# Optimization experiments

Measured on AMD Instinct MI355X. Metric: run time of the kernel, lower is better.

## Reference

```python
import jax, jax.numpy as jnp
import numpy as np

N_NODES = 100000
N_EDGES = 640000
D_IN = 128
HIDDEN = 256
OUT = 256
NUM_GRAPHS = 256


def setup_inputs() -> dict:
    key = jax.random.key(0)
    ks = jax.random.split(key, 8)
    x = jax.random.normal(ks[0], (N_NODES, D_IN), dtype=jnp.float32)
    edge_index = jax.random.randint(ks[1], (2, N_EDGES), 0, N_NODES, dtype=jnp.int64)
    batch = jnp.sort(jax.random.randint(ks[2], (N_NODES,), 0, NUM_GRAPHS, dtype=jnp.int64))
    s1 = 1.0 / np.sqrt(D_IN)
    s2 = 1.0 / np.sqrt(HIDDEN)
    W1_l = jax.random.normal(ks[3], (D_IN, HIDDEN), dtype=jnp.float32) * s1
    W1_r = jax.random.normal(ks[4], (D_IN, HIDDEN), dtype=jnp.float32) * s1
    b1 = jnp.zeros((HIDDEN,), dtype=jnp.float32)
    W2_l = jax.random.normal(ks[5], (HIDDEN, OUT), dtype=jnp.float32) * s2
    W2_r = jax.random.normal(ks[6], (HIDDEN, OUT), dtype=jnp.float32) * s2
    b2 = jnp.zeros((OUT,), dtype=jnp.float32)
    return {"x": x, "edge_index": edge_index, "batch": batch,
            "W1_l": W1_l, "b1": b1, "W1_r": W1_r,
            "W2_l": W2_l, "b2": b2, "W2_r": W2_r}


def _sage_conv(x, src, dst, W_l, b_l, W_r):
    # PyG SAGEConv, aggr='mean': lin_l(mean_{j in N(i)} x_j) + lin_r(x_i)
    n = x.shape[0]
    msgs = x[src]                                              # [E, d] gather
    agg = jax.ops.segment_sum(msgs, dst, num_segments=n)       # [N, d] scatter-add
    cnt = jax.ops.segment_sum(jnp.ones((src.shape[0],), x.dtype), dst, num_segments=n)
    mean = agg / jnp.maximum(cnt, 1.0)[:, None]
    return mean @ W_l + b_l + x @ W_r


def reference(x, edge_index, batch, W1_l, b1, W1_r, W2_l, b2, W2_r):
    src, dst = edge_index[0], edge_index[1]
    h = jax.nn.relu(_sage_conv(x, src, dst, W1_l, b1, W1_r))
    h = _sage_conv(h, src, dst, W2_l, b2, W2_r)
    # global_add_pool: segment sum over per-node graph ids
    return jax.ops.segment_sum(h, batch, num_segments=NUM_GRAPHS)  # [G, OUT]
```

## Files before the change

kernel.cpp:

```cpp
#include <hip/hip_runtime.h>

#define NN 100000
#define NE 640000
#define DIN 128
#define DH 256
#define DOUT 256
#define NG 256
#define NB1 ((NN + 255) / 256)

#define PECH 157
#define CPE (4 * PECH)
#define PEB ((NE + CPE - 1) / CPE)
#define GSP 8

#define PNB 1024
#define CHN2 ((NN + PNB - 1) / PNB)

#define BCH 4096
#define BNB ((NE + BCH - 1) / BCH)

typedef __bf16 bf16_t;
typedef __bf16 bf16x8 __attribute__((ext_vector_type(8)));
typedef __bf16 bf16x2 __attribute__((ext_vector_type(2)));
typedef float f32x4 __attribute__((ext_vector_type(4)));
typedef float f32v2 __attribute__((ext_vector_type(2)));

#if __has_builtin(__builtin_amdgcn_cvt_pk_fp8_f32) && __has_builtin(__builtin_amdgcn_cvt_pk_f32_fp8)
#define USE_HW_FP8 1
#else
#define USE_HW_FP8 0
#endif

#if !USE_HW_FP8
__device__ __forceinline__ unsigned f32_to_fp8_1(float f) {
  unsigned sg = (__float_as_uint(f) >> 31) << 7;
  float af = fabsf(f);
  unsigned body;
  if (af < 0.015625f) {
    body = (unsigned)(int)rintf(af * 512.0f);
  } else {
    unsigned bits = __float_as_uint(af);
    unsigned rb = bits + 0x7FFFFu + ((bits >> 20) & 1u);
    unsigned e = rb >> 23;
    body = ((e - 120u) << 3) | ((rb >> 20) & 7u);
  }
  return (sg | body) & 0xffu;
}
__device__ __forceinline__ float fp8_to_f32_1(unsigned b) {
  unsigned s = b >> 7, e = (b >> 3) & 15u, m = b & 7u;
  float v = (e == 0) ? (float)m * 0.001953125f
                     : __uint_as_float(((e + 120u) << 23) | (m << 20));
  return s ? -v : v;
}
#endif

__device__ __forceinline__ unsigned pack4_fp8(float v0, float v1, float v2, float v3) {
#if USE_HW_FP8
  int u = __builtin_amdgcn_cvt_pk_fp8_f32(v0, v1, 0, false);
  u = __builtin_amdgcn_cvt_pk_fp8_f32(v2, v3, u, true);
  return (unsigned)u;
#else
  return f32_to_fp8_1(v0) | (f32_to_fp8_1(v1) << 8) |
         (f32_to_fp8_1(v2) << 16) | (f32_to_fp8_1(v3) << 24);
#endif
}

__device__ __forceinline__ void unpack4_fp8(unsigned v, float* o) {
#if USE_HW_FP8
  f32v2 a = __builtin_amdgcn_cvt_pk_f32_fp8((int)v, false);
  f32v2 b = __builtin_amdgcn_cvt_pk_f32_fp8((int)v, true);
  o[0] = a[0]; o[1] = a[1]; o[2] = b[0]; o[3] = b[1];
#else
  o[0] = fp8_to_f32_1(v & 0xffu);         o[1] = fp8_to_f32_1((v >> 8) & 0xffu);
  o[2] = fp8_to_f32_1((v >> 16) & 0xffu); o[3] = fp8_to_f32_1(v >> 24);
#endif
}

__device__ __forceinline__ void unpack2_fp8(unsigned v, float* o) {
#if USE_HW_FP8
  f32v2 a = __builtin_amdgcn_cvt_pk_f32_fp8((int)v, false);
  o[0] = a[0]; o[1] = a[1];
#else
  o[0] = fp8_to_f32_1(v & 0xffu); o[1] = fp8_to_f32_1((v >> 8) & 0xffu);
#endif
}

__global__ void k_xcast(const float* __restrict__ x, bf16_t* __restrict__ xb,
                        unsigned char* __restrict__ xf8) {
  size_t i = ((size_t)blockIdx.x * 256 + threadIdx.x) * 8;
  if (i >= (size_t)NN * DIN) return;
  float4 a = *(const float4*)(x + i), b = *(const float4*)(x + i + 4);
  bf16x8 o;
  o[0] = (bf16_t)a.x; o[1] = (bf16_t)a.y; o[2] = (bf16_t)a.z; o[3] = (bf16_t)a.w;
  o[4] = (bf16_t)b.x; o[5] = (bf16_t)b.y; o[6] = (bf16_t)b.z; o[7] = (bf16_t)b.w;
  *(bf16x8*)(xb + i) = o;
  uint2 p;
  p.x = pack4_fp8(a.x, a.y, a.z, a.w);
  p.y = pack4_fp8(b.x, b.y, b.z, b.w);
  *(uint2*)(xf8 + i) = p;
}

__global__ void k_count(const int* __restrict__ dst, int* __restrict__ cnt) {
  int e = blockIdx.x * 256 + threadIdx.x;
  if (e < NE) atomicAdd(&cnt[dst[e]], 1);
}

__global__ void k_scan1(const int* __restrict__ cnt, int* __restrict__ rowptr,
                        int* __restrict__ part) {
  __shared__ int s[256];
  int t = threadIdx.x, i = blockIdx.x * 256 + t;
  int v = (i < NN) ? cnt[i] : 0;
  s[t] = v; __syncthreads();
#pragma unroll
  for (int off = 1; off < 256; off <<= 1) {
    int u = (t >= off) ? s[t - off] : 0;
    __syncthreads();
    s[t] += u;
    __syncthreads();
  }
  if (i < NN) rowptr[i] = s[t] - v;
  if (t == 255) part[blockIdx.x] = s[255];
}

__global__ void k_scan2(int* __restrict__ part) {
  __shared__ int s[512];
  int t = threadIdx.x;
  int v = (t < NB1) ? part[t] : 0;
  s[t] = v; __syncthreads();
#pragma unroll
  for (int off = 1; off < 512; off <<= 1) {
    int u = (t >= off) ? s[t - off] : 0;
    __syncthreads();
    s[t] += u;
    __syncthreads();
  }
  if (t < NB1) part[t] = s[t] - v;
}

__global__ void k_scan3(int* __restrict__ rowptr, const int* __restrict__ part) {
  int i = blockIdx.x * 256 + threadIdx.x;
  if (i < NN) rowptr[i] += part[i >> 8];
  if (i == 0) rowptr[NN] = NE;
}

__global__ void k_gstart2(const int* __restrict__ batch, const int* __restrict__ rowptr,
                          int* __restrict__ gstart, unsigned* __restrict__ wg) {
  int n = blockIdx.x * 256 + threadIdx.x;
  if (n >= NN) return;
  int b = batch[n];
  int prev = (n == 0) ? -1 : batch[n - 1];
  for (int g = prev + 1; g <= b; ++g) gstart[g] = n;
  if (n == NN - 1) {
    for (int g = b + 1; g <= NG; ++g) gstart[g] = NN;
  }
  int e0 = rowptr[n], e1 = rowptr[n + 1];
  unsigned val = ((unsigned)b << 16) | (unsigned)(e1 - e0);
  for (int e = e0; e < e1; ++e) wg[e] = val;
}

__global__ void k_bucket(const int* __restrict__ src, const int* __restrict__ dst,
                         const int* __restrict__ rowptr, int* __restrict__ fill,
                         int* __restrict__ col) {
  int cls = blockIdx.x & 7;
  int cb = blockIdx.x >> 3;
  int e0 = cb * BCH;
  int e1 = (e0 + BCH < NE) ? e0 + BCH : NE;
  for (int e = e0 + threadIdx.x; e < e1; e += 256) {
    int d = dst[e];
    if (((d >> 4) & 7) == cls) {
      int p = rowptr[d] + atomicAdd(&fill[d], 1);
      col[p] = src[e];
    }
  }
}

__global__ void k_agg1(const int* __restrict__ rowptr, const int* __restrict__ col,
                       const unsigned char* __restrict__ xf8, bf16_t* __restrict__ ag1) {
  int w = (blockIdx.x * 256 + threadIdx.x) >> 6;
  int lane = threadIdx.x & 63;
  if (w >= NN) return;
  w = __builtin_amdgcn_readfirstlane(w);
  int e0 = rowptr[w], e1 = rowptr[w + 1];
  float a0 = 0.f, a1 = 0.f;
  int e = e0;
  for (; e + 4 <= e1; e += 4) {
    int s0 = col[e], s1 = col[e + 1], s2 = col[e + 2], s3 = col[e + 3];
    unsigned v0 = *(const unsigned short*)(xf8 + (size_t)s0 * DIN + lane * 2);
    unsigned v1 = *(const unsigned short*)(xf8 + (size_t)s1 * DIN + lane * 2);
    unsigned v2 = *(const unsigned short*)(xf8 + (size_t)s2 * DIN + lane * 2);
    unsigned v3 = *(const unsigned short*)(xf8 + (size_t)s3 * DIN + lane * 2);
    float o[2];
    unpack2_fp8(v0, o); a0 += o[0]; a1 += o[1];
    unpack2_fp8(v1, o); a0 += o[0]; a1 += o[1];
    unpack2_fp8(v2, o); a0 += o[0]; a1 += o[1];
    unpack2_fp8(v3, o); a0 += o[0]; a1 += o[1];
  }
  for (; e < e1; ++e) {
    int s0 = col[e];
    unsigned v0 = *(const unsigned short*)(xf8 + (size_t)s0 * DIN + lane * 2);
    float o[2];
    unpack2_fp8(v0, o); a0 += o[0]; a1 += o[1];
  }
  float r = (e1 > e0) ? __builtin_amdgcn_rcpf((float)(e1 - e0)) : 0.f;
  bf16x2 ov;
  ov[0] = (bf16_t)(a0 * r); ov[1] = (bf16_t)(a1 * r);
  ((bf16x2*)ag1)[(size_t)w * 64 + lane] = ov;
}

__global__ void k_pack1(const float* __restrict__ Wl, const float* __restrict__ Wr,
                        bf16_t* __restrict__ Bp) {
  int t = blockIdx.x * 256 + threadIdx.x;
  if (t >= 8192) return;
  int lane = t & 63, nt = (t >> 6) & 15, kc = t >> 10;
  int n = nt * 16 + (lane & 15);
  int k0 = kc * 32 + (lane >> 4) * 8;
  bf16_t* o = Bp + ((size_t)(kc * 16 + nt) * 64 + lane) * 8;
  for (int j = 0; j < 8; ++j) {
    int k = k0 + j;
    float v = (k < 128) ? Wl[k * 256 + n] : Wr[(k - 128) * 256 + n];
    o[j] = (bf16_t)v;
  }
}

__launch_bounds__(256, 4)
__global__ void k_gemm1(const bf16_t* __restrict__ xb, const bf16_t* __restrict__ ag1,
                        const float* __restrict__ b1,
                        const bf16_t* __restrict__ Bp, unsigned char* __restrict__ hf8) {
  __shared__ unsigned char smem[64 * 512];
  int n0 = blockIdx.x * 64;
  int tid = threadIdx.x;
  {
    int row = tid >> 2, part = tid & 3;
    int node = n0 + row;
    unsigned sw = (row & 7) << 4;
    const uint4* ap = (const uint4*)(ag1 + (size_t)node * DIN);
    const uint4* xp = (const uint4*)(xb + (size_t)node * DIN);
#pragma unroll
    for (int i = 0; i < 4; ++i) {
      int mi = i * 4 + part;
      uint4 va = {0u, 0u, 0u, 0u}, vx = {0u, 0u, 0u, 0u};
      if (node < NN) { va = ap[mi]; vx = xp[mi]; }
      *(uint4*)(smem + row * 512 + (((unsigned)(mi * 16)) ^ sw)) = va;
      *(uint4*)(smem + row * 512 + ((unsigned)(256 + mi * 16) ^ sw)) = vx;
    }
  }
  __syncthreads();
  int wave = tid >> 6, lane = tid & 63, lhi = lane >> 4, llo = lane & 15;
  f32x4 acc[4][4] = {};
  const bf16x8* bptr = (const bf16x8*)Bp;
#pragma unroll
  for (int kc = 0; kc < 8; ++kc) {
    bf16x8 a[4], b[4];
#pragma unroll
    for (int mi = 0; mi < 4; ++mi) {
      int row = mi * 16 + llo;
      unsigned cb = ((unsigned)((kc * 32 + lhi * 8) * 2)) ^ ((row & 7) << 4);
      a[mi] = *(const bf16x8*)(smem + row * 512 + cb);
    }
#pragma unroll
    for (int ni = 0; ni < 4; ++ni)
      b[ni] = bptr[(kc * 16 + wave * 4 + ni) * 64 + lane];
#pragma unroll
    for (int mi = 0; mi < 4; ++mi)
#pragma unroll
      for (int ni = 0; ni < 4; ++ni)
        acc[mi][ni] = __builtin_amdgcn_mfma_f32_16x16x32_bf16(a[mi], b[ni], acc[mi][ni], 0, 0, 0);
  }
  float bias[4];
#pragma unroll
  for (int ni = 0; ni < 4; ++ni) bias[ni] = b1[wave * 64 + ni * 16 + llo];
#pragma unroll
  for (int mi = 0; mi < 4; ++mi)
#pragma unroll
    for (int j = 0; j < 4; ++j) {
      int node = n0 + mi * 16 + lhi * 4 + j;
      if (node < NN) {
        float v0 = fmaxf(acc[mi][0][j] + bias[0], 0.f);
        float v1 = fmaxf(acc[mi][1][j] + bias[1], 0.f);
        float v2 = fmaxf(acc[mi][2][j] + bias[2], 0.f);
        float v3 = fmaxf(acc[mi][3][j] + bias[3], 0.f);
        unsigned u = pack4_fp8(v0, v1, v2, v3);
        *(unsigned*)(hf8 + (size_t)node * 256 + wave * 64 + llo * 4) = u;
      }
    }
}

__global__ void k_poolE2(const int* __restrict__ col, const unsigned* __restrict__ wg,
                         const unsigned char* __restrict__ hf8, float* __restrict__ Y1) {
  __shared__ float gbuf[GSP][256];
  int tid = threadIdx.x;
  int c0 = blockIdx.x * CPE;
  int c1 = (c0 + CPE < NE) ? c0 + CPE : NE;
  if (c0 >= c1) return;
  int gmin = (int)(wg[c0] >> 16), gmax = (int)(wg[c1 - 1] >> 16);
  bool ldsok = (gmax - gmin) < GSP;
  for (int i = tid; i < GSP * 256; i += 256) (&gbuf[0][0])[i] = 0.f;
  __syncthreads();
  int wv = tid >> 6, lane = tid & 63;
  int e0 = __builtin_amdgcn_readfirstlane(c0 + wv * PECH);
  int e1 = e0 + PECH; if (e1 > c1) e1 = c1;
  int dmb = ((lane >> 4) << 6) | (lane & 15);
  float acc[4] = {0.f, 0.f, 0.f, 0.f};
  int curg = -1;
#define EFLUSH() do { if (curg >= 0) {                                        \
    if (ldsok) { float* gp = gbuf[curg - gmin];                               \
      atomicAdd(gp + (dmb | 0),  acc[0]); atomicAdd(gp + (dmb | 16), acc[1]); \
      atomicAdd(gp + (dmb | 32), acc[2]); atomicAdd(gp + (dmb | 48), acc[3]); \
    } else { float* yp = Y1 + (size_t)curg * 256;                             \
      unsafeAtomicAdd(yp + (dmb | 0),  acc[0]);                               \
      unsafeAtomicAdd(yp + (dmb | 16), acc[1]);                               \
      unsafeAtomicAdd(yp + (dmb | 32), acc[2]);                               \
      unsafeAtomicAdd(yp + (dmb | 48), acc[3]); }                             \
    acc[0] = acc[1] = acc[2] = acc[3] = 0.f; } } while (0)
  if (e0 < e1) {
    int e = e0;
    for (; e + 8 <= e1; e += 8) {
      int cv[8]; unsigned wvv[8]; unsigned hv[8];
#pragma unroll
      for (int i = 0; i < 8; ++i) { cv[i] = col[e + i]; wvv[i] = wg[e + i]; }
#pragma unroll
      for (int i = 0; i < 8; ++i)
        hv[i] = *(const unsigned*)(hf8 + (size_t)cv[i] * 256 + lane * 4);
#pragma unroll
      for (int i = 0; i < 8; ++i) {
        int g = (int)(wvv[i] >> 16);
        if (g != curg) { EFLUSH(); curg = g; }
        float w = __builtin_amdgcn_rcpf((float)(wvv[i] & 0xffffu));
        float o[4]; unpack4_fp8(hv[i], o);
        acc[0] += w * o[0]; acc[1] += w * o[1];
        acc[2] += w * o[2]; acc[3] += w * o[3];
      }
    }
    for (; e < e1; ++e) {
      int c = col[e]; unsigned wv2 = wg[e];
      unsigned hvv = *(const unsigned*)(hf8 + (size_t)c * 256 + lane * 4);
      int g = (int)(wv2 >> 16);
      if (g != curg) { EFLUSH(); curg = g; }
      float w = __builtin_amdgcn_rcpf((float)(wv2 & 0xffffu));
      float o[4]; unpack4_fp8(hvv, o);
      acc[0] += w * o[0]; acc[1] += w * o[1];
      acc[2] += w * o[2]; acc[3] += w * o[3];
    }
    EFLUSH();
  }
#undef EFLUSH
  __syncthreads();
  if (ldsok) {
    int ng = gmax - gmin + 1;
    for (int gi = 0; gi < ng; ++gi)
      unsafeAtomicAdd(&Y1[(size_t)(gmin + gi) * 256 + tid], gbuf[gi][tid]);
  }
}

__global__ void k_poolN(const int* __restrict__ batch, const unsigned char* __restrict__ hf8,
                        float* __restrict__ Y2) {
  __shared__ float gbuf[GSP][256];
  int tid = threadIdx.x;
  int n0 = blockIdx.x * CHN2;
  int n1 = (n0 + CHN2 < NN) ? n0 + CHN2 : NN;
  if (n0 >= n1) return;
  int gmin = batch[n0], gmax = batch[n1 - 1];
  bool ldsok = (gmax - gmin) < GSP;
  for (int i = tid; i < GSP * 256; i += 256) (&gbuf[0][0])[i] = 0.f;
  __syncthreads();
  int wv = tid >> 6, lane = tid & 63;
  const int per = (CHN2 + 3) >> 2;
  int a0 = n0 + wv * per;
  int a1 = a0 + per; if (a1 > n1) a1 = n1;
  int dmb = ((lane >> 4) << 6) | (lane & 15);
  float acc[4] = {0.f, 0.f, 0.f, 0.f};
  int curg = -1;
#define NFLUSH() do { if (curg >= 0) {                                        \
    if (ldsok) { float* gp = gbuf[curg - gmin];                               \
      atomicAdd(gp + (dmb | 0),  acc[0]); atomicAdd(gp + (dmb | 16), acc[1]); \
      atomicAdd(gp + (dmb | 32), acc[2]); atomicAdd(gp + (dmb | 48), acc[3]); \
    } else { float* yp = Y2 + (size_t)curg * 256;                             \
      unsafeAtomicAdd(yp + (dmb | 0),  acc[0]);                               \
      unsafeAtomicAdd(yp + (dmb | 16), acc[1]);                               \
      unsafeAtomicAdd(yp + (dmb | 32), acc[2]);                               \
      unsafeAtomicAdd(yp + (dmb | 48), acc[3]); }                             \
    acc[0] = acc[1] = acc[2] = acc[3] = 0.f; } } while (0)
  for (int n = a0; n < a1; ++n) {
    int g = batch[n];
    if (g != curg) { NFLUSH(); curg = g; }
    unsigned v = *(const unsigned*)(hf8 + (size_t)n * 256 + lane * 4);
    float o[4]; unpack4_fp8(v, o);
    acc[0] += o[0]; acc[1] += o[1]; acc[2] += o[2]; acc[3] += o[3];
  }
  NFLUSH();
#undef NFLUSH
  __syncthreads();
  if (ldsok) {
    int ng = gmax - gmin + 1;
    for (int gi = 0; gi < ng; ++gi)
      unsafeAtomicAdd(&Y2[(size_t)(gmin + gi) * 256 + tid], gbuf[gi][tid]);
  }
}

__global__ void k_out2(const float* __restrict__ Y1, const float* __restrict__ Y2,
                       const float* __restrict__ W2l, const float* __restrict__ W2r,
                       const float* __restrict__ b2, const int* __restrict__ gstart,
                       float* __restrict__ out) {
  __shared__ float ys[128];
  int g = blockIdx.x, ks = blockIdx.y, t = threadIdx.x;
  const float* Ysrc = (ks < 2) ? Y1 : Y2;
  const float* Wsrc = (ks < 2) ? W2l : W2r;
  int kbase = (ks & 1) * 128;
  if (t < 128) ys[t] = Ysrc[(size_t)g * 256 + kbase + t];
  __syncthreads();
  float s = 0.f;
  const float* wp = Wsrc + (size_t)kbase * 256 + t;
#pragma unroll 8
  for (int k = 0; k < 128; ++k) s += ys[k] * wp[(size_t)k * 256];
  if (ks == 0) {
    float cntf = (float)(gstart[g + 1] - gstart[g]);
    s += b2[t] * cntf;
  }
  unsafeAtomicAdd(&out[(size_t)g * 256 + t], s);
}

extern "C" void kernel_launch(void* const* d_in, const int* in_sizes, int n_in,
                              void* d_out, int out_size, void* d_ws, size_t ws_size,
                              hipStream_t stream) {
  const float* x   = (const float*)d_in[0];
  const int*   ei  = (const int*)d_in[1];
  const int*   bat = (const int*)d_in[2];
  const float* W1l = (const float*)d_in[3];
  const float* b1  = (const float*)d_in[4];
  const float* W1r = (const float*)d_in[5];
  const float* W2l = (const float*)d_in[6];
  const float* b2  = (const float*)d_in[7];
  const float* W2r = (const float*)d_in[8];
  const int* src = ei;
  const int* dst = ei + NE;

  char* ws = (char*)d_ws;
  size_t off = 0;
  int* cnt     = (int*)(ws + off); off += ((size_t)NN * 4 + 255) & ~(size_t)255;
  int* rowptr  = (int*)(ws + off); off += ((size_t)(NN + 1) * 4 + 255) & ~(size_t)255;
  int* part    = (int*)(ws + off); off += 512 * 4;
  int* fill    = (int*)(ws + off); off += ((size_t)NN * 4 + 255) & ~(size_t)255;
  int* gstart  = (int*)(ws + off); off += ((size_t)(NG + 1) * 4 + 255) & ~(size_t)255;
  int* col     = (int*)(ws + off); off += (size_t)NE * 4;
  unsigned* wg = (unsigned*)(ws + off); off += (size_t)NE * 4;
  bf16_t* Bp1  = (bf16_t*)(ws + off); off += (size_t)256 * 256 * 2;
  float* Y1    = (float*)(ws + off); off += (size_t)NG * 256 * 4;
  float* Y2    = (float*)(ws + off); off += (size_t)NG * 256 * 4;
  bf16_t* xb   = (bf16_t*)(ws + off); off += (size_t)NN * DIN * 2;
  unsigned char* xf8 = (unsigned char*)(ws + off); off += (size_t)NN * DIN;
  bf16_t* ag1  = (bf16_t*)(ws + off); off += (size_t)NN * DIN * 2;
  unsigned char* hf8 = (unsigned char*)(ws + off); off += (size_t)NN * DH;

  hipMemsetAsync(cnt, 0, (size_t)NN * 4, stream);
  hipMemsetAsync(fill, 0, (size_t)NN * 4, stream);
  hipMemsetAsync(Y1, 0, (size_t)NG * 256 * 4 * 2, stream);
  hipMemsetAsync(d_out, 0, (size_t)out_size * 4, stream);
  k_xcast<<<NN * DIN / 8 / 256, 256, 0, stream>>>(x, xb, xf8);
  k_pack1<<<32, 256, 0, stream>>>(W1l, W1r, Bp1);
  k_count<<<(NE + 255) / 256, 256, 0, stream>>>(dst, cnt);
  k_scan1<<<NB1, 256, 0, stream>>>(cnt, rowptr, part);
  k_scan2<<<1, 512, 0, stream>>>(part);
  k_scan3<<<NB1, 256, 0, stream>>>(rowptr, part);
  k_gstart2<<<NB1, 256, 0, stream>>>(bat, rowptr, gstart, wg);
  k_bucket<<<BNB * 8, 256, 0, stream>>>(src, dst, rowptr, fill, col);
  k_agg1<<<NN / 4, 256, 0, stream>>>(rowptr, col, xf8, ag1);
  k_gemm1<<<(NN + 63) / 64, 256, 0, stream>>>(xb, ag1, b1, Bp1, hf8);
  k_poolE2<<<PEB, 256, 0, stream>>>(col, wg, hf8, Y1);
  k_poolN<<<PNB, 256, 0, stream>>>(bat, hf8, Y2);
  k_out2<<<dim3(NG, 4), 256, 0, stream>>>(Y1, Y2, W2l, W2r, b2, gstart, (float*)d_out);
}
```

Before: 209.4 us.

## Store layer-1 inputs and aggregates in fp8, batch eight nodes per aggregation wave

The bf16 copy of x is dropped, and the mean aggregate is stored as fp8 instead of bf16. The GEMM now reads fp8 for both operands and converts them to bf16 in its shared-memory staging, which cuts the bytes written and read between the cast, aggregate and GEMM kernels. The aggregation kernel now processes eight consecutive nodes per wave over a flat edge range with 8-deep gather batching, and the edge pooling loop is unrolled to 16. The cost is extra fp8 quantisation error on x and on the aggregate, plus more conversion work inside the GEMM.

Measured after the change: 202.1 us. -3.5%, faster.

```diff
diff --git a/kernel.cpp b/kernel.cpp
--- a/kernel.cpp
+++ b/kernel.cpp
@@ -19,9 +19,12 @@
 #define BCH 4096
 #define BNB ((NE + BCH - 1) / BCH)
 
+#define ANW 8
+#define AGW ((NN + ANW - 1) / ANW)
+#define AGB ((AGW + 3) / 4)
+
 typedef __bf16 bf16_t;
 typedef __bf16 bf16x8 __attribute__((ext_vector_type(8)));
-typedef __bf16 bf16x2 __attribute__((ext_vector_type(2)));
 typedef float f32x4 __attribute__((ext_vector_type(4)));
 typedef float f32v2 __attribute__((ext_vector_type(2)));
 
@@ -65,6 +68,15 @@
 #endif
 }
 
+__device__ __forceinline__ unsigned short pack2_fp8(float v0, float v1) {
+#if USE_HW_FP8
+  int u = __builtin_amdgcn_cvt_pk_fp8_f32(v0, v1, 0, false);
+  return (unsigned short)(u & 0xffff);
+#else
+  return (unsigned short)(f32_to_fp8_1(v0) | (f32_to_fp8_1(v1) << 8));
+#endif
+}
+
 __device__ __forceinline__ void unpack4_fp8(unsigned v, float* o) {
 #if USE_HW_FP8
   f32v2 a = __builtin_amdgcn_cvt_pk_f32_fp8((int)v, false);
@@ -76,6 +88,11 @@
 #endif
 }
 
+__device__ __forceinline__ void unpack8_fp8(uint2 v, float* o) {
+  unpack4_fp8(v.x, o);
+  unpack4_fp8(v.y, o + 4);
+}
+
 __device__ __forceinline__ void unpack2_fp8(unsigned v, float* o) {
 #if USE_HW_FP8
   f32v2 a = __builtin_amdgcn_cvt_pk_f32_fp8((int)v, false);
@@ -85,15 +102,10 @@
 #endif
 }
 
-__global__ void k_xcast(const float* __restrict__ x, bf16_t* __restrict__ xb,
-                        unsigned char* __restrict__ xf8) {
+__global__ void k_xcast(const float* __restrict__ x, unsigned char* __restrict__ xf8) {
   size_t i = ((size_t)blockIdx.x * 256 + threadIdx.x) * 8;
   if (i >= (size_t)NN * DIN) return;
   float4 a = *(const float4*)(x + i), b = *(const float4*)(x + i + 4);
-  bf16x8 o;
-  o[0] = (bf16_t)a.x; o[1] = (bf16_t)a.y; o[2] = (bf16_t)a.z; o[3] = (bf16_t)a.w;
-  o[4] = (bf16_t)b.x; o[5] = (bf16_t)b.y; o[6] = (bf16_t)b.z; o[7] = (bf16_t)b.w;
-  *(bf16x8*)(xb + i) = o;
   uint2 p;
   p.x = pack4_fp8(a.x, a.y, a.z, a.w);
   p.y = pack4_fp8(b.x, b.y, b.z, b.w);
@@ -175,36 +187,55 @@
 }
 
 __global__ void k_agg1(const int* __restrict__ rowptr, const int* __restrict__ col,
-                       const unsigned char* __restrict__ xf8, bf16_t* __restrict__ ag1) {
-  int w = (blockIdx.x * 256 + threadIdx.x) >> 6;
+                       const unsigned char* __restrict__ xf8, unsigned char* __restrict__ ag1f8) {
+  int wid = (blockIdx.x * 256 + threadIdx.x) >> 6;
   int lane = threadIdx.x & 63;
-  if (w >= NN) return;
-  w = __builtin_amdgcn_readfirstlane(w);
-  int e0 = rowptr[w], e1 = rowptr[w + 1];
+  int n0 = wid * ANW;
+  if (n0 >= NN) return;
+  int n1 = n0 + ANW; if (n1 > NN) n1 = NN;
+  int e = rowptr[n0];
+  int eTot = rowptr[n1];
+  int n = n0;
+  int estart = e;
+  int eend = rowptr[n0 + 1];
   float a0 = 0.f, a1 = 0.f;
-  int e = e0;
-  for (; e + 4 <= e1; e += 4) {
-    int s0 = col[e], s1 = col[e + 1], s2 = col[e + 2], s3 = col[e + 3];
-    unsigned v0 = *(const unsigned short*)(xf8 + (size_t)s0 * DIN + lane * 2);
-    unsigned v1 = *(const unsigned short*)(xf8 + (size_t)s1 * DIN + lane * 2);
-    unsigned v2 = *(const unsigned short*)(xf8 + (size_t)s2 * DIN + lane * 2);
-    unsigned v3 = *(const unsigned short*)(xf8 + (size_t)s3 * DIN + lane * 2);
+#define AFLUSH()                                                              \
+  do {                                                                        \
+    float r = (eend > estart) ? __builtin_amdgcn_rcpf((float)(eend - estart)) \
+                              : 0.f;                                          \
+    *(unsigned short*)(ag1f8 + (size_t)n * DIN + lane * 2) =                  \
+        pack2_fp8(a0 * r, a1 * r);                                            \
+    a0 = 0.f; a1 = 0.f;                                                       \
+    estart = eend; n++;                                                       \
+    if (n < n1) eend = rowptr[n + 1];                                         \
+  } while (0)
+  while (e + 8 <= eTot) {
+    unsigned v[8];
+#pragma unroll
+    for (int i = 0; i < 8; ++i) {
+      int s = col[e + i];
+      v[i] = *(const unsigned short*)(xf8 + (size_t)s * DIN + lane * 2);
+    }
+#pragma unroll
+    for (int i = 0; i < 8; ++i) {
+      while (e + i >= eend) AFLUSH();
+      float o[2];
+      unpack2_fp8(v[i], o);
+      a0 += o[0]; a1 += o[1];
+    }
+    e += 8;
+  }
+  while (e < eTot) {
+    int s = col[e];
+    unsigned v = *(const unsigned short*)(xf8 + (size_t)s * DIN + lane * 2);
+    while (e >= eend) AFLUSH();
     float o[2];
-    unpack2_fp8(v0, o); a0 += o[0]; a1 += o[1];
-    unpack2_fp8(v1, o); a0 += o[0]; a1 += o[1];
-    unpack2_fp8(v2, o); a0 += o[0]; a1 += o[1];
-    unpack2_fp8(v3, o); a0 += o[0]; a1 += o[1];
-  }
-  for (; e < e1; ++e) {
-    int s0 = col[e];
-    unsigned v0 = *(const unsigned short*)(xf8 + (size_t)s0 * DIN + lane * 2);
-    float o[2];
-    unpack2_fp8(v0, o); a0 += o[0]; a1 += o[1];
-  }
-  float r = (e1 > e0) ? __builtin_amdgcn_rcpf((float)(e1 - e0)) : 0.f;
-  bf16x2 ov;
-  ov[0] = (bf16_t)(a0 * r); ov[1] = (bf16_t)(a1 * r);
-  ((bf16x2*)ag1)[(size_t)w * 64 + lane] = ov;
+    unpack2_fp8(v, o);
+    a0 += o[0]; a1 += o[1];
+    ++e;
+  }
+  while (n < n1) AFLUSH();
+#undef AFLUSH
 }
 
 __global__ void k_pack1(const float* __restrict__ Wl, const float* __restrict__ Wr,
@@ -223,7 +254,8 @@
 }
 
 __launch_bounds__(256, 4)
-__global__ void k_gemm1(const bf16_t* __restrict__ xb, const bf16_t* __restrict__ ag1,
+__global__ void k_gemm1(const unsigned char* __restrict__ xf8,
+                        const unsigned char* __restrict__ ag1f8,
                         const float* __restrict__ b1,
                         const bf16_t* __restrict__ Bp, unsigned char* __restrict__ hf8) {
   __shared__ unsigned char smem[64 * 512];
@@ -233,15 +265,21 @@
     int row = tid >> 2, part = tid & 3;
     int node = n0 + row;
     unsigned sw = (row & 7) << 4;
-    const uint4* ap = (const uint4*)(ag1 + (size_t)node * DIN);
-    const uint4* xp = (const uint4*)(xb + (size_t)node * DIN);
+    const uint2* ap = (const uint2*)(ag1f8 + (size_t)node * DIN);
+    const uint2* xp = (const uint2*)(xf8 + (size_t)node * DIN);
 #pragma unroll
     for (int i = 0; i < 4; ++i) {
       int mi = i * 4 + part;
-      uint4 va = {0u, 0u, 0u, 0u}, vx = {0u, 0u, 0u, 0u};
+      uint2 va = {0u, 0u}, vx = {0u, 0u};
       if (node < NN) { va = ap[mi]; vx = xp[mi]; }
-      *(uint4*)(smem + row * 512 + (((unsigned)(mi * 16)) ^ sw)) = va;
-      *(uint4*)(smem + row * 512 + ((unsigned)(256 + mi * 16) ^ sw)) = vx;
+      float oa[8], ox[8];
+      unpack8_fp8(va, oa);
+      unpack8_fp8(vx, ox);
+      bf16x8 wa, wx;
+#pragma unroll
+      for (int j = 0; j < 8; ++j) { wa[j] = (bf16_t)oa[j]; wx[j] = (bf16_t)ox[j]; }
+      *(bf16x8*)(smem + row * 512 + (((unsigned)(mi * 16)) ^ sw)) = wa;
+      *(bf16x8*)(smem + row * 512 + ((unsigned)(256 + mi * 16) ^ sw)) = wx;
     }
   }
   __syncthreads();
@@ -314,15 +352,16 @@
     acc[0] = acc[1] = acc[2] = acc[3] = 0.f; } } while (0)
   if (e0 < e1) {
     int e = e0;
-    for (; e + 8 <= e1; e += 8) {
-      int cv[8]; unsigned wvv[8]; unsigned hv[8];
-#pragma unroll
-      for (int i = 0; i < 8; ++i) { cv[i] = col[e + i]; wvv[i] = wg[e + i]; }
-#pragma unroll
-      for (int i = 0; i < 8; ++i)
-        hv[i] = *(const unsigned*)(hf8 + (size_t)cv[i] * 256 + lane * 4);
-#pragma unroll
-      for (int i = 0; i < 8; ++i) {
+    for (; e + 16 <= e1; e += 16) {
+      unsigned wvv[16]; unsigned hv[16];
+#pragma unroll
+      for (int i = 0; i < 16; ++i) {
+        int c = col[e + i];
+        wvv[i] = wg[e + i];
+        hv[i] = *(const unsigned*)(hf8 + (size_t)c * 256 + lane * 4);
+      }
+#pragma unroll
+      for (int i = 0; i < 16; ++i) {
         int g = (int)(wvv[i] >> 16);
         if (g != curg) { EFLUSH(); curg = g; }
         float w = __builtin_amdgcn_rcpf((float)(wvv[i] & 0xffffu));
@@ -446,16 +485,15 @@
   bf16_t* Bp1  = (bf16_t*)(ws + off); off += (size_t)256 * 256 * 2;
   float* Y1    = (float*)(ws + off); off += (size_t)NG * 256 * 4;
   float* Y2    = (float*)(ws + off); off += (size_t)NG * 256 * 4;
-  bf16_t* xb   = (bf16_t*)(ws + off); off += (size_t)NN * DIN * 2;
   unsigned char* xf8 = (unsigned char*)(ws + off); off += (size_t)NN * DIN;
-  bf16_t* ag1  = (bf16_t*)(ws + off); off += (size_t)NN * DIN * 2;
+  unsigned char* ag1f8 = (unsigned char*)(ws + off); off += (size_t)NN * DIN;
   unsigned char* hf8 = (unsigned char*)(ws + off); off += (size_t)NN * DH;
 
   hipMemsetAsync(cnt, 0, (size_t)NN * 4, stream);
   hipMemsetAsync(fill, 0, (size_t)NN * 4, stream);
   hipMemsetAsync(Y1, 0, (size_t)NG * 256 * 4 * 2, stream);
   hipMemsetAsync(d_out, 0, (size_t)out_size * 4, stream);
-  k_xcast<<<NN * DIN / 8 / 256, 256, 0, stream>>>(x, xb, xf8);
+  k_xcast<<<NN * DIN / 8 / 256, 256, 0, stream>>>(x, xf8);
   k_pack1<<<32, 256, 0, stream>>>(W1l, W1r, Bp1);
   k_count<<<(NE + 255) / 256, 256, 0, stream>>>(dst, cnt);
   k_scan1<<<NB1, 256, 0, stream>>>(cnt, rowptr, part);
@@ -463,8 +501,8 @@
   k_scan3<<<NB1, 256, 0, stream>>>(rowptr, part);
   k_gstart2<<<NB1, 256, 0, stream>>>(bat, rowptr, gstart, wg);
   k_bucket<<<BNB * 8, 256, 0, stream>>>(src, dst, rowptr, fill, col);
-  k_agg1<<<NN / 4, 256, 0, stream>>>(rowptr, col, xf8, ag1);
-  k_gemm1<<<(NN + 63) / 64, 256, 0, stream>>>(xb, ag1, b1, Bp1, hf8);
+  k_agg1<<<AGB, 256, 0, stream>>>(rowptr, col, xf8, ag1f8);
+  k_gemm1<<<(NN + 63) / 64, 256, 0, stream>>>(xf8, ag1f8, b1, Bp1, hf8);
   k_poolE2<<<PEB, 256, 0, stream>>>(col, wg, hf8, Y1);
   k_poolN<<<PNB, 256, 0, stream>>>(bat, hf8, Y2);
   k_out2<<<dim3(NG, 4), 256, 0, stream>>>(Y1, Y2, W2l, W2r, b2, gstart, (float*)d_out);
```
